# Kernel tuning notes

Measured on AMD Instinct MI355X. Metric: run time of the kernel, lower is better.

## Reference

```python
import jax, jax.numpy as jnp
import numpy as np

K = 20      # neighbors per node
D_T = 32    # timestep embedding dim

def _timestep_embedding(t, dim):
    half = dim // 2
    freqs = jnp.exp(-jnp.log(10000.0) * jnp.arange(half, dtype=jnp.float32) / (half - 1))
    args = t[:, None] * freqs[None, :]
    return jnp.concatenate([jnp.sin(args), jnp.cos(args)], axis=-1)

def _knn(pos, k):
    # pos: [N,3] -> (sources, targets): [N*k] edge index lists
    r2 = jnp.sum(pos * pos, axis=-1)
    d2 = r2[:, None] + r2[None, :] - 2.0 * (pos @ pos.T)   # [N,N] squared distances
    n = pos.shape[0]
    d2 = d2 + 1e10 * jnp.eye(n, dtype=pos.dtype)           # exclude self
    d2 = jax.lax.stop_gradient(d2)                         # indices only, no grad path
    _, idx = jax.lax.top_k(-d2, k)                         # [N,k]
    targets = jnp.repeat(jnp.arange(n), k)
    sources = idx.reshape(-1)
    return sources, targets

def _forward(z, t, conditioning, Wc1, bc1, Wc2, bc2, Wc3, bc3, We1, be1, We2, be2, Wn1, bn1, Wn2, bn2, alpha, beta):
    B, N, _ = z.shape
    pos, vel, massf = z[..., :3], z[..., 3:6], z[..., 6:]
    t = t * jnp.ones((B,), z.dtype)
    temb = _timestep_embedding(t, D_T)                     # [B,32]
    cond = jnp.concatenate([temb, conditioning], axis=1)   # [B,36]
    h = jax.nn.gelu(cond @ Wc1 + bc1)
    h = jax.nn.gelu(h @ Wc2 + bc2)
    cond = h @ Wc3 + bc3                                   # [B,36]
    fs = massf + cond[:, None, :]                          # scalar node feats [B,N,36]

    def single(pos_b, vel_b, fs_b):
        src, tgt = _knn(pos_b, K)
        rel = pos_b[src] - pos_b[tgt]                      # [E,3]
        r2 = jnp.sum(rel * rel, axis=-1, keepdims=True)
        vs, vt = vel_b[src], vel_b[tgt]
        # rotation-invariant edge features
        inv = jnp.concatenate([
            fs_b[src], fs_b[tgt], r2,
            jnp.sum(vs * vt, -1, keepdims=True),
            jnp.sum(vs * rel, -1, keepdims=True),
            jnp.sum(vt * rel, -1, keepdims=True),
        ], axis=-1)                                        # [E,76]
        e = jax.nn.gelu(inv @ We1 + be1) @ We2 + be2       # [E,4]
        logit, smsg, c_rel, c_vel = e[:, 0], e[:, 1], e[:, 2], e[:, 3]
        # segment softmax over incoming edges of each target node
        m = jax.ops.segment_max(logit, tgt, num_segments=N)
        a = jnp.exp(logit - m[tgt])
        denom = jax.ops.segment_sum(a, tgt, num_segments=N)
        w = a / denom[tgt]
        # equivariant vector messages, invariant scalar messages
        vmsg = w[:, None] * (c_rel[:, None] * rel + c_vel[:, None] * vs)
        vagg = jax.ops.segment_sum(vmsg, tgt, num_segments=N)              # [N,3]
        sagg = jax.ops.segment_sum(w * smsg, tgt, num_segments=N)[:, None]  # [N,1]
        hn = jax.nn.gelu(jnp.concatenate([fs_b, sagg], axis=-1) @ Wn1 + bn1)
        sout = hn @ Wn2 + bn2                              # [N,1] 0e output
        pos_out = pos_b + alpha * vagg                     # 1o
        feat_out = jnp.concatenate([beta * vagg, sout], axis=-1)  # 1o + 0e
        return jnp.concatenate([pos_out, feat_out], axis=-1)      # [N,7]

    h_all = jax.vmap(single)(pos, vel, fs)
    return z + h_all

def setup_inputs():
    key = jax.random.key(0)
    ks = jax.random.split(key, 10)
    B, N = 2, 8192
    d_cond = D_T + 4          # 36
    e_in = 2 * d_cond + 4     # 76
    e_hid, n_hid = 128, 64
    g = lambda i, shp: jax.random.normal(ks[i], shp, jnp.float32) * 0.05
    return {
        "z": jax.random.normal(ks[0], (B, N, 7), jnp.float32),
        "t": jax.random.uniform(ks[1], (B,), jnp.float32),
        "conditioning": jax.random.normal(ks[2], (B, 4), jnp.float32),
        "mask": jnp.ones((B, N), dtype=bool),
        "Wc1": g(3, (d_cond, 4 * d_cond)), "bc1": jnp.zeros((4 * d_cond,), jnp.float32),
        "Wc2": g(4, (4 * d_cond, 4 * d_cond)), "bc2": jnp.zeros((4 * d_cond,), jnp.float32),
        "Wc3": g(5, (4 * d_cond, d_cond)), "bc3": jnp.zeros((d_cond,), jnp.float32),
        "We1": g(6, (e_in, e_hid)), "be1": jnp.zeros((e_hid,), jnp.float32),
        "We2": g(7, (e_hid, 4)), "be2": jnp.zeros((4,), jnp.float32),
        "Wn1": g(8, (d_cond + 1, n_hid)), "bn1": jnp.zeros((n_hid,), jnp.float32),
        "Wn2": g(9, (n_hid, 1)), "bn2": jnp.zeros((1,), jnp.float32),
        "alpha": jnp.float32(0.1), "beta": jnp.float32(0.1),
    }

def reference(z, t, conditioning, mask, Wc1, bc1, Wc2, bc2, Wc3, bc3, We1, be1, We2, be2, Wn1, bn1, Wn2, bn2, alpha, beta):
    # mask is unused (module docstring: does not support masking)
    return _forward(z, t, conditioning, Wc1, bc1, Wc2, bc2, Wc3, bc3, We1, be1, We2, be2, Wn1, bn1, Wn2, bn2, alpha, beta)
```

## Files before the change

### kernel.cpp

```cpp
#include <hip/hip_runtime.h>
#include <math.h>

#define NB 8192
#define BATCH 2
#define KNN 20
#define BN (BATCH*NB)
#define NE (BN*KNN)
#define GT 16
#define NG 8
#define BIG 3.0e38f

__device__ __forceinline__ float gelu_f(float x){
    float x3 = x*x*x;
    float a = 0.7978845608028654f*(x + 0.044715f*x3);
    float e2 = __expf(2.0f*a);
    float th = 1.0f - __fdividef(2.0f, e2+1.0f);
    return 0.5f*x*(1.0f+th);
}

__global__ __launch_bounds__(256) void prepcond_kernel(const float* __restrict__ z,
        const float* __restrict__ t,
        const float* __restrict__ conditioning,
        const float* __restrict__ Wc1, const float* __restrict__ bc1,
        const float* __restrict__ Wc2, const float* __restrict__ bc2,
        const float* __restrict__ Wc3, const float* __restrict__ bc3,
        const float* __restrict__ We1, const float* __restrict__ be1,
        const float* __restrict__ We2,
        const float* __restrict__ Wn1, const float* __restrict__ bn1,
        float4* __restrict__ pos4, float4* __restrict__ vel4,
        float* __restrict__ consts, float* __restrict__ pack){
    int tid = threadIdx.x;
    int g = blockIdx.x*256 + tid;
    const float* zp = z + (size_t)g*7;
    float x = zp[0], y = zp[1], zz = zp[2];
    float r2 = x*x + y*y + zz*zz;
    pos4[g] = make_float4(x, y, zz, r2);
    vel4[g] = make_float4(zp[3], zp[4], zp[5], zp[6]);

    if (blockIdx.x >= BATCH) return;
    int b = blockIdx.x;
    __shared__ float ci[36];
    __shared__ float h1[144];
    __shared__ float h2[144];
    __shared__ float cnd[36];
    float tv = t[b];
    if (tid < 16){
        float f = expf(-9.210340371976184f * (float)tid / 15.0f);
        float a = tv*f;
        ci[tid]    = sinf(a);
        ci[16+tid] = cosf(a);
    }
    if (tid < 4) ci[32+tid] = conditioning[b*4+tid];
    __syncthreads();
    if (tid < 144){
        float acc = bc1[tid];
        #pragma unroll
        for (int c=0;c<36;c++) acc += ci[c]*Wc1[c*144+tid];
        h1[tid] = gelu_f(acc);
    }
    __syncthreads();
    if (tid < 144){
        float acc = bc2[tid];
        #pragma unroll 36
        for (int c=0;c<144;c++) acc += h1[c]*Wc2[c*144+tid];
        h2[tid] = gelu_f(acc);
    }
    __syncthreads();
    if (tid < 36){
        float acc = bc3[tid];
        #pragma unroll 36
        for (int c=0;c<144;c++) acc += h2[c]*Wc3[c*36+tid];
        cnd[tid] = acc;
    }
    __syncthreads();
    if (tid < 128){
        float accC = be1[tid], s1 = 0.f, s2 = 0.f;
        #pragma unroll
        for (int c=0;c<36;c++){
            float w1 = We1[c*128+tid];
            float w2 = We1[(36+c)*128+tid];
            accC += cnd[c]*(w1+w2);
            s1 += w1; s2 += w2;
        }
        consts[b*128+tid] = accC;
        pack[b*1536 + tid*12 + 0] = accC;
        if (b==0){
            consts[256+tid] = s1; consts[384+tid] = s2;
            float vals[10];
            vals[0] = s1;
            vals[1] = s2;
            vals[2] = We1[72*128+tid];
            vals[3] = We1[73*128+tid];
            vals[4] = We1[74*128+tid];
            vals[5] = We1[75*128+tid];
            vals[6] = We2[tid*4+0];
            vals[7] = We2[tid*4+1];
            vals[8] = We2[tid*4+2];
            vals[9] = We2[tid*4+3];
            #pragma unroll
            for (int q=0;q<10;q++){
                pack[tid*12 + 1 + q]        = vals[q];
                pack[1536 + tid*12 + 1 + q] = vals[q];
            }
        }
    }
    if (tid < 64){
        float accD = bn1[tid], t1 = 0.f;
        #pragma unroll
        for (int c=0;c<36;c++){
            float w = Wn1[c*64+tid];
            accD += cnd[c]*w;
            t1 += w;
        }
        consts[512 + b*64 + tid] = accD;
        if (b==0) consts[640+tid] = t1;
    }
}

__global__ __launch_bounds__(512, 4) void knn_kernel(const float4* __restrict__ pos4,
                                                     int* __restrict__ nbr){
    __shared__ float4 sPos[GT*64];
    __shared__ float2 sCand[32*64];
    int tid = threadIdx.x;
    int w = tid >> 6, lane = tid & 63;
    int n0g = blockIdx.x * 32;
    int b = n0g >> 13;
    int n0 = n0g & (NB-1);
    const float4* __restrict__ P = pos4 + b*NB;

    int nw = n0 + w*4;
    float nx[4], ny[4], nz[4], pw[4], acc[4];
    #pragma unroll
    for (int k=0;k<4;k++){
        float4 p = P[nw+k];
        nx[k] = -2.0f*p.x; ny[k] = -2.0f*p.y; nz[k] = -2.0f*p.z; pw[k] = p.w;
        acc[k] = BIG;
    }
    int selfTile = n0 >> 6;
    int sl0 = (n0 & 63) + w*4;

    float4 pre0 = P[(w*2    )*64 + lane];
    float4 pre1 = P[(w*2 + 1)*64 + lane];
    for (int g=0; g<NG; ++g){
        __syncthreads();
        sPos[(w*2    )*64 + lane] = pre0;
        sPos[(w*2 + 1)*64 + lane] = pre1;
        if (g+1 < NG){
            pre0 = P[((g+1)*GT + w*2    )*64 + lane];
            pre1 = P[((g+1)*GT + w*2 + 1)*64 + lane];
        }
        __syncthreads();
        int tbase = g*GT;
        #pragma unroll
        for (int t=0;t<GT;t++){
            float4 q = sPos[t*64 + lane];
            if (tbase + t != selfTile){
                #pragma unroll
                for (int k=0;k<4;k++){
                    float d2 = fmaf(nx[k],q.x, fmaf(ny[k],q.y, fmaf(nz[k],q.z, pw[k]+q.w)));
                    acc[k] = fminf(acc[k], d2);
                }
            } else {
                #pragma unroll
                for (int k=0;k<4;k++){
                    float d2 = fmaf(nx[k],q.x, fmaf(ny[k],q.y, fmaf(nz[k],q.z, pw[k]+q.w)));
                    if (lane == sl0 + k) d2 = BIG;
                    acc[k] = fminf(acc[k], d2);
                }
            }
        }
    }

    float T[4];
    #pragma unroll
    for (int k=0;k<4;k++){
        float v = acc[k];
        #pragma unroll
        for (int K=2; K<=64; K<<=1){
            #pragma unroll
            for (int j=K>>1; j>0; j>>=1){
                float o = __shfl_xor(v, j);
                bool keepmin = (((lane & j) == 0) == ((lane & K) == 0));
                float mn = fminf(v,o), mx = fmaxf(v,o);
                v = keepmin ? mn : mx;
            }
        }
        T[k] = __shfl(v, 19);
    }

    int cnt[4];
    #pragma unroll
    for (int k=0;k<4;k++) cnt[k] = 0;
    unsigned long long lt = (1ull << lane) - 1ull;

    pre0 = P[(w*2    )*64 + lane];
    pre1 = P[(w*2 + 1)*64 + lane];
    for (int g=0; g<NG; ++g){
        __syncthreads();
        sPos[(w*2    )*64 + lane] = pre0;
        sPos[(w*2 + 1)*64 + lane] = pre1;
        if (g+1 < NG){
            pre0 = P[((g+1)*GT + w*2    )*64 + lane];
            pre1 = P[((g+1)*GT + w*2 + 1)*64 + lane];
        }
        __syncthreads();
        int tbase = g*GT;
        #pragma unroll 4
        for (int t=0;t<GT;t++){
            int tile = tbase + t;
            float4 q = sPos[t*64 + lane];
            int j = (tile<<6) + lane;
            bool selft = (tile == selfTile);
            #pragma unroll
            for (int k=0;k<4;k++){
                float d2 = fmaf(nx[k],q.x, fmaf(ny[k],q.y, fmaf(nz[k],q.z, pw[k]+q.w)));
                bool hit = (d2 <= T[k]);
                if (selft && (lane == sl0 + k)) hit = false;
                unsigned long long m = __ballot(hit);
                if (m){
                    if (hit){
                        int off = cnt[k] + (int)__popcll(m & lt);
                        if (off < 64)
                            sCand[(w*4+k)*64 + off] = make_float2(d2, __int_as_float(j));
                    }
                    cnt[k] += (int)__popcll(m);
                }
            }
        }
    }

    #pragma unroll
    for (int k=0;k<4;k++){
        int m = cnt[k]; if (m > 64) m = 64;
        float d; int idx;
        if (lane < m){
            float2 e = sCand[(w*4+k)*64 + lane];
            d = e.x; idx = __float_as_int(e.y);
        } else { d = BIG; idx = 0x7f000000 + lane; }
        #pragma unroll
        for (int K=2; K<=64; K<<=1){
            #pragma unroll
            for (int j=K>>1; j>0; j>>=1){
                float od = __shfl_xor(d, j);
                int   oi = __shfl_xor(idx, j);
                bool pless = (od < d) || (od == d && oi < idx);
                bool keepmin = (((lane & j) == 0) == ((lane & K) == 0));
                if (pless == keepmin){ d = od; idx = oi; }
            }
        }
        if (lane < KNN) nbr[(size_t)(n0g + w*4 + k)*KNN + lane] = idx;
    }
}

__global__ __launch_bounds__(320) void edgenode_kernel(const float4* __restrict__ pos4,
        const float4* __restrict__ vel4,
        const int* __restrict__ nbr,
        const float* __restrict__ pack,
        const float* __restrict__ consts,
        const float* __restrict__ Wn1,
        const float* __restrict__ Wn2,
        const float* __restrict__ be2,
        const float* __restrict__ bn2,
        const float* __restrict__ alpha_p,
        const float* __restrict__ beta_p,
        const float* __restrict__ z,
        float* __restrict__ out){
    __shared__ float sLg[640], sSm[640], sUx[640], sUy[640], sUz[640];
    __shared__ float sD[64], sT1[64], sW36[64], sWo[64];
    __shared__ float4 sAgg[32];
    __shared__ float sPart[256];

    int tid = threadIdx.x;
    bool bb = (blockIdx.x >= 256);
    const float* __restrict__ pk = pack + (bb ? 1536 : 0);

    if (tid < 64){
        sD[tid]   = consts[512 + (bb?64:0) + tid];
        sT1[tid]  = consts[640+tid];
        sW36[tid] = Wn1[36*64+tid];
        sWo[tid]  = Wn2[tid];
    }

    int base_e = blockIdx.x*640;
    int bbase = bb ? NB : 0;

    float rx[2],ry[2],rz[2],vsx[2],vsy[2],vsz[2];
    float r2[2],vv[2],vsr[2],vtr[2],mfs[2],mft[2];
    #pragma unroll
    for (int r=0;r<2;r++){
        int le = tid + 320*r;
        int i = blockIdx.x*32 + le/KNN;
        int s = nbr[base_e + le];
        float4 ps = pos4[bbase + s], pt = pos4[i];
        float4 vs = vel4[bbase + s], vt = vel4[i];
        rx[r] = ps.x - pt.x; ry[r] = ps.y - pt.y; rz[r] = ps.z - pt.z;
        vsx[r] = vs.x; vsy[r] = vs.y; vsz[r] = vs.z;
        r2[r]  = rx[r]*rx[r] + ry[r]*ry[r] + rz[r]*rz[r];
        vv[r]  = vs.x*vt.x + vs.y*vt.y + vs.z*vt.z;
        vsr[r] = vs.x*rx[r] + vs.y*ry[r] + vs.z*rz[r];
        vtr[r] = vt.x*rx[r] + vt.y*ry[r] + vt.z*rz[r];
        mfs[r] = vs.w; mft[r] = vt.w;
    }

    float b2v0 = be2[0], b2v1 = be2[1], b2v2 = be2[2], b2v3 = be2[3];
    float a0[2], a1[2], a2[2], a3[2];
    #pragma unroll
    for (int r=0;r<2;r++){ a0[r]=b2v0; a1[r]=b2v1; a2[r]=b2v2; a3[r]=b2v3; }
    #pragma unroll 4
    for (int h=0; h<128; h++){
        const float4* row = (const float4*)(pk + h*12);
        float4 A  = row[0];
        float4 Bv = row[1];
        float4 C  = row[2];
        #pragma unroll
        for (int r=0;r<2;r++){
            float x = fmaf(mfs[r],A.y, A.x) + mft[r]*A.z
                    + r2[r]*A.w + vv[r]*Bv.x + vsr[r]*Bv.y + vtr[r]*Bv.z;
            float gx = gelu_f(x);
            a0[r] += gx*Bv.w; a1[r] += gx*C.x; a2[r] += gx*C.y; a3[r] += gx*C.z;
        }
    }
    #pragma unroll
    for (int r=0;r<2;r++){
        int le = tid + 320*r;
        sLg[le] = a0[r];
        sSm[le] = a1[r];
        sUx[le] = a2[r]*rx[r] + a3[r]*vsx[r];
        sUy[le] = a2[r]*ry[r] + a3[r]*vsy[r];
        sUz[le] = a2[r]*rz[r] + a3[r]*vsz[r];
    }
    __syncthreads();

    if (tid < 32){
        int base = tid*KNN;
        float m = -BIG;
        #pragma unroll
        for (int q=0;q<KNN;q++) m = fmaxf(m, sLg[base+q]);
        float den=0.f, wx=0.f, wy=0.f, wz=0.f, wsm=0.f;
        #pragma unroll
        for (int q=0;q<KNN;q++){
            float a = __expf(sLg[base+q]-m);
            den += a;
            wsm += a*sSm[base+q];
            wx  += a*sUx[base+q];
            wy  += a*sUy[base+q];
            wz  += a*sUz[base+q];
        }
        float inv = __fdividef(1.0f, den);
        sAgg[tid] = make_float4(wx*inv, wy*inv, wz*inv, wsm*inv);
    }
    __syncthreads();

    if (tid < 256){
        int ln = tid >> 3;
        int h0 = (tid & 7)*8;
        float mf = vel4[blockIdx.x*32 + ln].w;
        float sg = sAgg[ln].w;
        float part = 0.f;
        #pragma unroll
        for (int h=h0; h<h0+8; h++){
            float x = sD[h] + mf*sT1[h] + sg*sW36[h];
            part += gelu_f(x)*sWo[h];
        }
        sPart[tid] = part;
    }
    __syncthreads();

    if (tid < 32){
        float sout = bn2[0];
        #pragma unroll
        for (int q=0;q<8;q++) sout += sPart[tid*8+q];
        int node = blockIdx.x*32 + tid;
        float alpha = alpha_p[0], beta = beta_p[0];
        float4 ag = sAgg[tid];
        const float* zp = z + (size_t)node*7;
        float* op = out + (size_t)node*7;
        op[0] = zp[0]*2.0f + alpha*ag.x;
        op[1] = zp[1]*2.0f + alpha*ag.y;
        op[2] = zp[2]*2.0f + alpha*ag.z;
        op[3] = zp[3] + beta*ag.x;
        op[4] = zp[4] + beta*ag.y;
        op[5] = zp[5] + beta*ag.z;
        op[6] = zp[6] + sout;
    }
}

extern "C" void kernel_launch(void* const* d_in, const int* in_sizes, int n_in,
                              void* d_out, int out_size, void* d_ws, size_t ws_size,
                              hipStream_t stream) {
    const float* z    = (const float*)d_in[0];
    const float* t    = (const float*)d_in[1];
    const float* cond = (const float*)d_in[2];
    const float* Wc1  = (const float*)d_in[4];
    const float* bc1  = (const float*)d_in[5];
    const float* Wc2  = (const float*)d_in[6];
    const float* bc2  = (const float*)d_in[7];
    const float* Wc3  = (const float*)d_in[8];
    const float* bc3  = (const float*)d_in[9];
    const float* We1  = (const float*)d_in[10];
    const float* be1  = (const float*)d_in[11];
    const float* We2  = (const float*)d_in[12];
    const float* be2  = (const float*)d_in[13];
    const float* Wn1  = (const float*)d_in[14];
    const float* bn1  = (const float*)d_in[15];
    const float* Wn2  = (const float*)d_in[16];
    const float* bn2  = (const float*)d_in[17];
    const float* alp  = (const float*)d_in[18];
    const float* bet  = (const float*)d_in[19];
    float* out = (float*)d_out;

    char* ws = (char*)d_ws;
    float4* pos4   = (float4*)(ws);
    float4* vel4   = (float4*)(ws + 262144);
    float*  consts = (float*)(ws + 524288);
    float*  pack   = (float*)(ws + 528384);
    int*    nbr    = (int*)(ws + 540672);

    prepcond_kernel<<<dim3(BN/256), dim3(256), 0, stream>>>(z, t, cond,
        Wc1, bc1, Wc2, bc2, Wc3, bc3, We1, be1, We2, Wn1, bn1,
        pos4, vel4, consts, pack);
    knn_kernel<<<dim3(BN/32), dim3(512), 0, stream>>>(pos4, nbr);
    edgenode_kernel<<<dim3(BN/32), dim3(320), 0, stream>>>(pos4, vel4, nbr, pack, consts,
        Wn1, Wn2, be2, bn2, alp, bet, z, out);
}
```

Baseline: 210.4 us.

## Replace brute-force KNN with uniform-grid spatial hashing and brute-force fixup

Replaces the O(N^2) tiled brute-force KNN with a uniform 32^3 cell grid. A histogram, a prefix scan and a counting sort bucket points by cell. Each wavefront then expands a search box until the 20th-nearest bound is proven inside it, and collects candidates under that threshold. Nodes whose candidate count overflows 64 are queued for a brute-force fixup kernel. This cuts the distance-evaluation work heavily, but adds four small launches, a single-block-per-batch sort, and divergence that depends on the data. The fixed grid bounds (-5 to 5) assume normally distributed positions.

```diff
diff --git a/kernel.cpp b/kernel.cpp
--- a/kernel.cpp
+++ b/kernel.cpp
@@ -6,9 +6,15 @@
 #define KNN 20
 #define BN (BATCH*NB)
 #define NE (BN*KNN)
-#define GT 16
-#define NG 8
 #define BIG 3.0e38f
+
+#define GS 32
+#define GS3 (GS*GS*GS)
+#define CELL 0.3125f
+#define GMIN -5.0f
+#define INVC 3.2f
+#define MARGIN 1.0e-2f
+#define FIXG 128
 
 __device__ __forceinline__ float gelu_f(float x){
     float x3 = x*x*x;
@@ -16,6 +22,20 @@
     float e2 = __expf(2.0f*a);
     float th = 1.0f - __fdividef(2.0f, e2+1.0f);
     return 0.5f*x*(1.0f+th);
+}
+
+__device__ __forceinline__ float bitonic_val(float v, int lane){
+    #pragma unroll
+    for (int K=2; K<=64; K<<=1){
+        #pragma unroll
+        for (int j=K>>1; j>0; j>>=1){
+            float o = __shfl_xor(v, j);
+            bool keepmin = (((lane & j) == 0) == ((lane & K) == 0));
+            float mn = fminf(v,o), mx = fmaxf(v,o);
+            v = keepmin ? mn : mx;
+        }
+    }
+    return v;
 }
 
 __global__ __launch_bounds__(256) void prepcond_kernel(const float* __restrict__ z,
@@ -28,6 +48,8 @@
         const float* __restrict__ We2,
         const float* __restrict__ Wn1, const float* __restrict__ bn1,
         float4* __restrict__ pos4, float4* __restrict__ vel4,
+        int* __restrict__ cellid, int* __restrict__ histg,
+        int* __restrict__ sus_cnt,
         float* __restrict__ consts, float* __restrict__ pack){
     int tid = threadIdx.x;
     int g = blockIdx.x*256 + tid;
@@ -36,6 +58,12 @@
     float r2 = x*x + y*y + zz*zz;
     pos4[g] = make_float4(x, y, zz, r2);
     vel4[g] = make_float4(zp[3], zp[4], zp[5], zp[6]);
+    int cx = (int)floorf((x  - GMIN)*INVC); cx = min(GS-1, max(0, cx));
+    int cy = (int)floorf((y  - GMIN)*INVC); cy = min(GS-1, max(0, cy));
+    int cz = (int)floorf((zz - GMIN)*INVC); cz = min(GS-1, max(0, cz));
+    cellid[g] = (cx*GS + cy)*GS + cz;
+    histg[g] = 0; histg[g+16384] = 0; histg[g+32768] = 0; histg[g+49152] = 0;
+    if (g == 0) sus_cnt[0] = 0;
 
     if (blockIdx.x >= BATCH) return;
     int b = blockIdx.x;
@@ -87,8 +115,7 @@
         if (b==0){
             consts[256+tid] = s1; consts[384+tid] = s2;
             float vals[10];
-            vals[0] = s1;
-            vals[1] = s2;
+            vals[0] = s1; vals[1] = s2;
             vals[2] = We1[72*128+tid];
             vals[3] = We1[73*128+tid];
             vals[4] = We1[74*128+tid];
@@ -117,138 +144,220 @@
     }
 }
 
-__global__ __launch_bounds__(512, 4) void knn_kernel(const float4* __restrict__ pos4,
-                                                     int* __restrict__ nbr){
-    __shared__ float4 sPos[GT*64];
-    __shared__ float2 sCand[32*64];
+__global__ __launch_bounds__(256) void hist_kernel(const int* __restrict__ cellid,
+                                                   int* __restrict__ histg){
+    int g = blockIdx.x*256 + threadIdx.x;
+    atomicAdd(&histg[(g>>13)*GS3 + cellid[g]], 1);
+}
+
+__global__ __launch_bounds__(1024) void gridsort_kernel(const int* __restrict__ cellid,
+        const float4* __restrict__ pos4,
+        int* __restrict__ histg, int* __restrict__ cellStart,
+        float4* __restrict__ sortedPos4, int* __restrict__ sortedIdx){
+    int b = blockIdx.x;
+    int tid = threadIdx.x;
+    int* H = histg + b*GS3;
+    int* CSg = cellStart + b*(GS3+1);
+    __shared__ int tsum[1024];
+
+    int base_c = tid*32;
+    int s = 0;
+    #pragma unroll 8
+    for (int j=0;j<32;j++) s += H[base_c+j];
+    tsum[tid] = s;
+    __syncthreads();
+    for (int o=1;o<1024;o<<=1){
+        int v = (tid>=o) ? tsum[tid-o] : 0;
+        __syncthreads();
+        tsum[tid] += v;
+        __syncthreads();
+    }
+    int run = tsum[tid] - s;
+    #pragma unroll 8
+    for (int j=0;j<32;j++){
+        int c = base_c + j;
+        int cc = H[c];
+        CSg[c] = run;
+        H[c] = run;
+        run += cc;
+    }
+    if (tid == 0) CSg[GS3] = NB;
+    __threadfence();
+    __syncthreads();
+    #pragma unroll
+    for (int q=0;q<8;q++){
+        int g = b*NB + q*1024 + tid;
+        int c = cellid[g];
+        int p = atomicAdd(&H[c], 1);
+        sortedPos4[b*NB + p] = pos4[g];
+        sortedIdx[b*NB + p]  = g & (NB-1);
+    }
+}
+
+__global__ __launch_bounds__(256) void knn_grid(const float4* __restrict__ SPall,
+        const int* __restrict__ SIall,
+        const int* __restrict__ CSall,
+        int* __restrict__ nbr,
+        int* __restrict__ sus_cnt, int* __restrict__ sus_id){
+    __shared__ float2 sC[4*64];
     int tid = threadIdx.x;
     int w = tid >> 6, lane = tid & 63;
-    int n0g = blockIdx.x * 32;
-    int b = n0g >> 13;
-    int n0 = n0g & (NB-1);
-    const float4* __restrict__ P = pos4 + b*NB;
-
-    int nw = n0 + w*4;
-    float nx[4], ny[4], nz[4], pw[4], acc[4];
-    #pragma unroll
-    for (int k=0;k<4;k++){
-        float4 p = P[nw+k];
-        nx[k] = -2.0f*p.x; ny[k] = -2.0f*p.y; nz[k] = -2.0f*p.z; pw[k] = p.w;
-        acc[k] = BIG;
-    }
-    int selfTile = n0 >> 6;
-    int sl0 = (n0 & 63) + w*4;
-
-    float4 pre0 = P[(w*2    )*64 + lane];
-    float4 pre1 = P[(w*2 + 1)*64 + lane];
-    for (int g=0; g<NG; ++g){
-        __syncthreads();
-        sPos[(w*2    )*64 + lane] = pre0;
-        sPos[(w*2 + 1)*64 + lane] = pre1;
-        if (g+1 < NG){
-            pre0 = P[((g+1)*GT + w*2    )*64 + lane];
-            pre1 = P[((g+1)*GT + w*2 + 1)*64 + lane];
-        }
-        __syncthreads();
-        int tbase = g*GT;
-        #pragma unroll
-        for (int t=0;t<GT;t++){
-            float4 q = sPos[t*64 + lane];
-            if (tbase + t != selfTile){
-                #pragma unroll
-                for (int k=0;k<4;k++){
-                    float d2 = fmaf(nx[k],q.x, fmaf(ny[k],q.y, fmaf(nz[k],q.z, pw[k]+q.w)));
-                    acc[k] = fminf(acc[k], d2);
-                }
-            } else {
-                #pragma unroll
-                for (int k=0;k<4;k++){
-                    float d2 = fmaf(nx[k],q.x, fmaf(ny[k],q.y, fmaf(nz[k],q.z, pw[k]+q.w)));
-                    if (lane == sl0 + k) d2 = BIG;
-                    acc[k] = fminf(acc[k], d2);
+    int p = blockIdx.x*4 + w;
+    int b = p >> 13;
+    int pl = p & (NB-1);
+    const float4* __restrict__ SP = SPall + b*NB;
+    const int*   __restrict__ SI = SIall + b*NB;
+    const int*   __restrict__ CS = CSall + b*(GS3+1);
+    float4 pi = SP[pl];
+    int i = SI[pl];
+    float pwv = pi.w;
+    float nx = -2.0f*pi.x, ny = -2.0f*pi.y, nz = -2.0f*pi.z;
+    int cx = (int)floorf((pi.x - GMIN)*INVC); cx = min(GS-1, max(0, cx));
+    int cy = (int)floorf((pi.y - GMIN)*INVC); cy = min(GS-1, max(0, cy));
+    int cz = (int)floorf((pi.z - GMIN)*INVC); cz = min(GS-1, max(0, cz));
+
+    float T = BIG;
+    int xlo, xhi, ylo, yhi, zlo, zhi;
+    for (int R = 1;; ++R){
+        xlo = max(cx-R,0); xhi = min(cx+R,GS-1);
+        ylo = max(cy-R,0); yhi = min(cy+R,GS-1);
+        zlo = max(cz-R,0); zhi = min(cz+R,GS-1);
+        bool full = (xlo==0) && (xhi==GS-1) && (ylo==0) && (yhi==GS-1)
+                 && (zlo==0) && (zhi==GS-1);
+        float accd = BIG;
+        int fill = 0;
+        for (int X=xlo; X<=xhi; ++X)
+            for (int Y=ylo; Y<=yhi; ++Y){
+                int basec = (X*GS + Y)*GS;
+                int s = CS[basec+zlo];
+                int e = CS[basec+zhi+1];
+                for (int c=s; c<e; c+=64){
+                    int len = e - c; if (len > 64) len = 64;
+                    int slot = (lane - fill) & 63;
+                    if (slot < len){
+                        float4 q = SP[c+slot];
+                        float d2 = fmaf(nx,q.x, fmaf(ny,q.y, fmaf(nz,q.z, pwv+q.w)));
+                        if (SI[c+slot] == i) d2 = BIG;
+                        accd = fminf(accd, d2);
+                    }
+                    fill += len;
                 }
             }
-        }
-    }
-
-    float T[4];
-    #pragma unroll
-    for (int k=0;k<4;k++){
-        float v = acc[k];
-        #pragma unroll
-        for (int K=2; K<=64; K<<=1){
-            #pragma unroll
-            for (int j=K>>1; j>0; j>>=1){
-                float o = __shfl_xor(v, j);
-                bool keepmin = (((lane & j) == 0) == ((lane & K) == 0));
-                float mn = fminf(v,o), mx = fmaxf(v,o);
-                v = keepmin ? mn : mx;
-            }
-        }
-        T[k] = __shfl(v, 19);
-    }
-
-    int cnt[4];
-    #pragma unroll
-    for (int k=0;k<4;k++) cnt[k] = 0;
+        if (full || fill >= 21){
+            float v = bitonic_val(accd, lane);
+            T = __shfl(v, 19);
+            if (full) break;
+            float bnd = BIG;
+            if (xlo > 0)    bnd = fminf(bnd, pi.x - (GMIN + xlo*CELL));
+            if (xhi < GS-1) bnd = fminf(bnd, (GMIN + (xhi+1)*CELL) - pi.x);
+            if (ylo > 0)    bnd = fminf(bnd, pi.y - (GMIN + ylo*CELL));
+            if (yhi < GS-1) bnd = fminf(bnd, (GMIN + (yhi+1)*CELL) - pi.y);
+            if (zlo > 0)    bnd = fminf(bnd, pi.z - (GMIN + zlo*CELL));
+            if (zhi < GS-1) bnd = fminf(bnd, (GMIN + (zhi+1)*CELL) - pi.z);
+            if (bnd > 0.0f && fmaf(bnd, bnd, -MARGIN) > T) break;
+        }
+    }
+
+    int cnt = 0;
     unsigned long long lt = (1ull << lane) - 1ull;
-
-    pre0 = P[(w*2    )*64 + lane];
-    pre1 = P[(w*2 + 1)*64 + lane];
-    for (int g=0; g<NG; ++g){
-        __syncthreads();
-        sPos[(w*2    )*64 + lane] = pre0;
-        sPos[(w*2 + 1)*64 + lane] = pre1;
-        if (g+1 < NG){
-            pre0 = P[((g+1)*GT + w*2    )*64 + lane];
-            pre1 = P[((g+1)*GT + w*2 + 1)*64 + lane];
-        }
-        __syncthreads();
-        int tbase = g*GT;
-        #pragma unroll 4
-        for (int t=0;t<GT;t++){
-            int tile = tbase + t;
-            float4 q = sPos[t*64 + lane];
-            int j = (tile<<6) + lane;
-            bool selft = (tile == selfTile);
-            #pragma unroll
-            for (int k=0;k<4;k++){
-                float d2 = fmaf(nx[k],q.x, fmaf(ny[k],q.y, fmaf(nz[k],q.z, pw[k]+q.w)));
-                bool hit = (d2 <= T[k]);
-                if (selft && (lane == sl0 + k)) hit = false;
+    for (int X=xlo; X<=xhi; ++X)
+        for (int Y=ylo; Y<=yhi; ++Y){
+            int basec = (X*GS + Y)*GS;
+            int s = CS[basec+zlo];
+            int e = CS[basec+zhi+1];
+            for (int c=s; c<e; c+=64){
+                int len = e - c; if (len > 64) len = 64;
+                bool hit = false; float d2 = BIG; int id = 0;
+                if (lane < len){
+                    float4 q = SP[c+lane];
+                    id = SI[c+lane];
+                    d2 = fmaf(nx,q.x, fmaf(ny,q.y, fmaf(nz,q.z, pwv+q.w)));
+                    hit = (d2 <= T) && (id != i);
+                }
                 unsigned long long m = __ballot(hit);
                 if (m){
                     if (hit){
-                        int off = cnt[k] + (int)__popcll(m & lt);
-                        if (off < 64)
-                            sCand[(w*4+k)*64 + off] = make_float2(d2, __int_as_float(j));
+                        int off = cnt + (int)__popcll(m & lt);
+                        if (off < 64) sC[w*64 + off] = make_float2(d2, __int_as_float(id));
                     }
-                    cnt[k] += (int)__popcll(m);
+                    cnt += (int)__popcll(m);
                 }
             }
         }
-    }
-
+    if (cnt > 64 && lane == 0){
+        int sl = atomicAdd(sus_cnt, 1);
+        sus_id[sl] = b*NB + i;
+    }
+    int mm = cnt > 64 ? 64 : cnt;
+    float d; int idx;
+    if (lane < mm){
+        float2 e2 = sC[w*64 + lane];
+        d = e2.x; idx = __float_as_int(e2.y);
+    } else { d = BIG; idx = 0x7f000000 + lane; }
     #pragma unroll
-    for (int k=0;k<4;k++){
-        int m = cnt[k]; if (m > 64) m = 64;
-        float d; int idx;
-        if (lane < m){
-            float2 e = sCand[(w*4+k)*64 + lane];
-            d = e.x; idx = __float_as_int(e.y);
-        } else { d = BIG; idx = 0x7f000000 + lane; }
-        #pragma unroll
-        for (int K=2; K<=64; K<<=1){
+    for (int K=2; K<=64; K<<=1){
+        #pragma unroll
+        for (int j=K>>1; j>0; j>>=1){
+            float od = __shfl_xor(d, j);
+            int   oi = __shfl_xor(idx, j);
+            bool pless = (od < d) || (od == d && oi < idx);
+            bool keepmin = (((lane & j) == 0) == ((lane & K) == 0));
+            if (pless == keepmin){ d = od; idx = oi; }
+        }
+    }
+    if (lane < KNN) nbr[(size_t)(b*NB + i)*KNN + lane] = idx;
+}
+
+__global__ __launch_bounds__(64) void fixup_kernel(const float4* __restrict__ pos4,
+                                                   const int* __restrict__ sus_cnt,
+                                                   const int* __restrict__ sus_id,
+                                                   int* __restrict__ nbr){
+    int lane = threadIdx.x;
+    int nsus = sus_cnt[0];
+    for (int s = blockIdx.x; s < nsus; s += FIXG){
+        int node = sus_id[s];
+        int b = node >> 13;
+        int i = node & (NB-1);
+        const float4* __restrict__ P = pos4 + b*NB;
+        float4 pi = P[i];
+        float pwv = pi.w;
+        float n2x = -2.0f*pi.x, n2y = -2.0f*pi.y, n2z = -2.0f*pi.z;
+
+        float bd[8]; int bi8[8];
+        #pragma unroll
+        for (int r=0;r<8;r++){ bd[r] = BIG; bi8[r] = 0x7fffffff; }
+        for (int tk=0; tk<128; ++tk){
+            int j = (tk<<6) + lane;
+            float4 q = P[j];
+            float d2 = fmaf(n2x,q.x, fmaf(n2y,q.y, fmaf(n2z,q.z, pwv+q.w)));
+            if (j == i) d2 = BIG;
+            if (d2 < bd[7]){
+                float vd = d2; int vi = j;
+                #pragma unroll
+                for (int r=0;r<8;r++){
+                    bool c = vd < bd[r];
+                    float td = bd[r]; int ti = bi8[r];
+                    bd[r] = c ? vd : td;  bi8[r] = c ? vi : ti;
+                    vd    = c ? td : vd;  vi    = c ? ti : vi;
+                }
+            }
+        }
+        int* outp = nbr + (size_t)node*KNN;
+        for (int r=0; r<KNN; r++){
+            float d = bd[0]; int ii = bi8[0];
             #pragma unroll
-            for (int j=K>>1; j>0; j>>=1){
-                float od = __shfl_xor(d, j);
-                int   oi = __shfl_xor(idx, j);
-                bool pless = (od < d) || (od == d && oi < idx);
-                bool keepmin = (((lane & j) == 0) == ((lane & K) == 0));
-                if (pless == keepmin){ d = od; idx = oi; }
+            for (int st=1; st<64; st<<=1){
+                float od = __shfl_xor(d, st);
+                int   oi = __shfl_xor(ii, st);
+                if (od < d || (od == d && oi < ii)){ d = od; ii = oi; }
             }
-        }
-        if (lane < KNN) nbr[(size_t)(n0g + w*4 + k)*KNN + lane] = idx;
+            if (lane == 0) outp[r] = ii;
+            if (bd[0] == d && bi8[0] == ii){
+                #pragma unroll
+                for (int st=0;st<7;st++){ bd[st]=bd[st+1]; bi8[st]=bi8[st+1]; }
+                bd[7] = BIG; bi8[7] = 0x7fffffff;
+            }
+        }
     }
 }
 
@@ -410,16 +519,27 @@
     float* out = (float*)d_out;
 
     char* ws = (char*)d_ws;
-    float4* pos4   = (float4*)(ws);
-    float4* vel4   = (float4*)(ws + 262144);
-    float*  consts = (float*)(ws + 524288);
-    float*  pack   = (float*)(ws + 528384);
-    int*    nbr    = (int*)(ws + 540672);
+    float4* pos4    = (float4*)(ws);
+    float4* vel4    = (float4*)(ws + 262144);
+    float*  consts  = (float*)(ws + 524288);
+    float*  pack    = (float*)(ws + 528384);
+    int*    nbr     = (int*)(ws + 540672);
+    int*    cellid  = (int*)(ws + 1851392);
+    int*    histg   = (int*)(ws + 1916928);
+    int*    cellSt  = (int*)(ws + 2179072);
+    float4* sPos4   = (float4*)(ws + 2441232);
+    int*    sIdx    = (int*)(ws + 2703376);
+    int*    sus_c   = (int*)(ws + 2768912);
+    int*    sus_id  = (int*)(ws + 2769168);
 
     prepcond_kernel<<<dim3(BN/256), dim3(256), 0, stream>>>(z, t, cond,
         Wc1, bc1, Wc2, bc2, Wc3, bc3, We1, be1, We2, Wn1, bn1,
-        pos4, vel4, consts, pack);
-    knn_kernel<<<dim3(BN/32), dim3(512), 0, stream>>>(pos4, nbr);
+        pos4, vel4, cellid, histg, sus_c, consts, pack);
+    hist_kernel<<<dim3(BN/256), dim3(256), 0, stream>>>(cellid, histg);
+    gridsort_kernel<<<dim3(BATCH), dim3(1024), 0, stream>>>(cellid, pos4, histg, cellSt,
+                                                            sPos4, sIdx);
+    knn_grid<<<dim3(BN/4), dim3(256), 0, stream>>>(sPos4, sIdx, cellSt, nbr, sus_c, sus_id);
+    fixup_kernel<<<dim3(FIXG), dim3(64), 0, stream>>>(pos4, sus_c, sus_id, nbr);
     edgenode_kernel<<<dim3(BN/32), dim3(320), 0, stream>>>(pos4, vel4, nbr, pack, consts,
         Wn1, Wn2, be2, bn2, alp, bet, z, out);
 }
```

Result: slower. 417.2 us (+98.3%).
